# Kernel tuning notes

Hardware: AMD Instinct MI355X
Metric: run time of the kernel (lower is better)

Reference implementation:

```python
import jax, jax.numpy as jnp
import numpy as np

USER_NUM = 100000
ITEM_NUM = 50000
N_NODES = USER_NUM + ITEM_NUM
EMB = 64
LAYERS = 3
NNZ = 2400000


def spmm(rows, cols, vals, x, n):
    # sparse [n, n] (COO) @ dense [n, d] -> [n, d]
    gathered = vals[:, None] * x[cols]          # [nnz, d]
    return jax.ops.segment_sum(gathered, rows, num_segments=n)


def setup_inputs() -> dict:
    key = jax.random.key(0)
    ks = jax.random.split(key, 7)
    return {
        "user_emb": jax.random.normal(ks[0], (USER_NUM, EMB), jnp.float32) * 0.1,
        "item_emb": jax.random.normal(ks[1], (ITEM_NUM, EMB), jnp.float32) * 0.1,
        "w1": jax.random.normal(ks[2], (LAYERS, EMB, EMB), jnp.float32) * (1.0 / np.sqrt(EMB)),
        "w2": jax.random.normal(ks[3], (LAYERS, EMB, EMB), jnp.float32) * (1.0 / np.sqrt(EMB)),
        "adj_vals": jax.random.uniform(ks[4], (NNZ,), jnp.float32) * (1.0 / 16.0),
        "adj_rows": jax.random.randint(ks[5], (NNZ,), 0, N_NODES, jnp.int32),
        "adj_cols": jax.random.randint(ks[6], (NNZ,), 0, N_NODES, jnp.int32),
    }


def reference(user_emb, item_emb, w1, w2, adj_vals, adj_rows, adj_cols):
    ego = jnp.concatenate([user_emb, item_emb], axis=0)   # [N, d]
    n = ego.shape[0]
    all_emb = [ego]
    for k in range(w1.shape[0]):
        temp = ego @ w1[k]                                # [N, d]
        agg_temp = spmm(adj_rows, adj_cols, adj_vals, temp, n)
        agg_ego = spmm(adj_rows, adj_cols, adj_vals, ego, n)
        ego = jax.nn.leaky_relu(agg_temp + temp + (agg_ego * ego) @ w2[k])
        all_emb.append(ego)
    mean_emb = jnp.mean(jnp.stack(all_emb, axis=1), axis=1)  # [N, d]
    u = user_emb.shape[0]
    return mean_emb[:u], mean_emb[u:]
```

## Files before the change

kernel.cpp:

```cpp
#include <hip/hip_runtime.h>
#include <hip/hip_fp16.h>

typedef _Float16 f16;
typedef _Float16 f16x4 __attribute__((ext_vector_type(4)));
typedef _Float16 f16x8 __attribute__((ext_vector_type(8)));
typedef float f32x4 __attribute__((ext_vector_type(4)));

__device__ __forceinline__ float h2f(__half v) { return __half2float(v); }
__device__ __forceinline__ __half f2h(float v) { return __float2half(v); }

#define SCAN_CHUNK 2048
#define ASTRIDE 136

#define BSHIFT 8
#define BROWS (1 << BSHIFT)
#define MAXB 1024
#define TILE 4096
#define BCAP 5120

#define WT_ELEMS (64 * ASTRIDE)
#define WT_DWORDS (WT_ELEMS / 2)

__global__ void zero_out_kernel(float* __restrict__ out, int total) {
    int i = blockIdx.x * blockDim.x + threadIdx.x;
    if (i < total) out[i] = 0.0f;
}

__global__ void init_kernel(const float* __restrict__ user, const float* __restrict__ item,
                            __half* __restrict__ ego0, int usz, int total) {
    int i = blockIdx.x * blockDim.x + threadIdx.x;
    if (i >= total) return;
    float f = (i < usz) ? user[i] : item[i - usz];
    ego0[i] = f2h(f);
}

__global__ void wprep_kernel(const float* __restrict__ w1, const float* __restrict__ w2,
                             f16* __restrict__ wt_pre, int L) {
    int i = blockIdx.x * blockDim.x + threadIdx.x;
    int total = L * WT_ELEMS;
    if (i >= total) return;
    int layer = i / WT_ELEMS;
    int r = i % WT_ELEMS;
    int c = r / ASTRIDE, k = r % ASTRIDE;
    float v = 0.f;
    if (k < 64)       v = w1[(size_t)layer * 4096 + (size_t)k * 64 + c];
    else if (k < 128) v = w2[(size_t)layer * 4096 + (size_t)(k - 64) * 64 + c];
    wt_pre[i] = (f16)v;
}

__global__ void hist_kernel(const int* __restrict__ rows, int* __restrict__ cnt, int nnz) {
    int i = blockIdx.x * blockDim.x + threadIdx.x;
    if (i < nnz) atomicAdd(&cnt[rows[i]], 1);
}

__global__ void scan_pass1(const int* __restrict__ cnt, int* __restrict__ bsum, int n) {
    __shared__ int wt[4];
    int tid = threadIdx.x;
    int base = blockIdx.x * SCAN_CHUNK + tid * 8;
    int s = 0;
    #pragma unroll
    for (int k = 0; k < 8; ++k) { int i = base + k; if (i < n) s += cnt[i]; }
    #pragma unroll
    for (int o = 32; o > 0; o >>= 1) s += __shfl_down(s, o, 64);
    int lane = tid & 63, wid = tid >> 6;
    if (lane == 0) wt[wid] = s;
    __syncthreads();
    if (tid == 0) bsum[blockIdx.x] = wt[0] + wt[1] + wt[2] + wt[3];
}

__global__ void scan_pass2(int* __restrict__ bsum, int nb, int* __restrict__ total) {
    if (threadIdx.x == 0) {
        int run = 0;
        for (int b = 0; b < nb; ++b) { int v = bsum[b]; bsum[b] = run; run += v; }
        *total = run;
    }
}

__global__ void scan_pass3(int* __restrict__ cnt, const int* __restrict__ bsum,
                           int* __restrict__ rptr, int n, const int* __restrict__ total) {
    __shared__ int wt[4];
    int tid = threadIdx.x;
    int base = blockIdx.x * SCAN_CHUNK + tid * 8;
    int v[8];
    int s = 0;
    #pragma unroll
    for (int k = 0; k < 8; ++k) { int i = base + k; v[k] = (i < n) ? cnt[i] : 0; s += v[k]; }
    int lane = tid & 63, wid = tid >> 6;
    int xs = s;
    #pragma unroll
    for (int o = 1; o < 64; o <<= 1) { int t = __shfl_up(xs, o, 64); if (lane >= o) xs += t; }
    if (lane == 63) wt[wid] = xs;
    __syncthreads();
    int wexcl = 0;
    for (int w = 0; w < wid; ++w) wexcl += wt[w];
    int run = bsum[blockIdx.x] + wexcl + (xs - s);
    #pragma unroll
    for (int k = 0; k < 8; ++k) {
        int i = base + k;
        if (i < n) { rptr[i] = run; cnt[i] = run; }
        run += v[k];
    }
    if (blockIdx.x == 0 && tid == 0) rptr[n] = *total;
}

__global__ void scatter_kernel(const int* __restrict__ rows, const int* __restrict__ cols,
                               const float* __restrict__ vals, int* __restrict__ cursor,
                               int2* __restrict__ edges, int nnz) {
    int i = blockIdx.x * blockDim.x + threadIdx.x;
    if (i >= nnz) return;
    int r = rows[i];
    int pos = atomicAdd(&cursor[r], 1);
    edges[pos] = make_int2(cols[i], __float_as_int(vals[i]));
}

__global__ __launch_bounds__(256)
void bhist_kernel(const int* __restrict__ rows, int* __restrict__ bcnt, int nnz, int nbuck) {
    __shared__ int hist[MAXB];
    int tid = threadIdx.x;
    for (int j = tid; j < nbuck; j += 256) hist[j] = 0;
    __syncthreads();
    int i = blockIdx.x * TILE + tid;
    #pragma unroll
    for (int k = 0; k < 16; ++k, i += 256)
        if (i < nnz) atomicAdd(&hist[rows[i] >> BSHIFT], 1);
    __syncthreads();
    for (int j = tid; j < nbuck; j += 256)
        if (hist[j]) atomicAdd(&bcnt[j], hist[j]);
}

__global__ void bscan_kernel(const int* __restrict__ bcnt, int* __restrict__ bbase,
                             int* __restrict__ gcur, int nbuck) {
    if (threadIdx.x == 0) {
        int run = 0;
        for (int b = 0; b < nbuck; ++b) { bbase[b] = run; gcur[b] = run; run += bcnt[b]; }
        bbase[nbuck] = run;
    }
}

__global__ __launch_bounds__(256)
void binA_kernel(const int* __restrict__ rows, const int* __restrict__ cols,
                 const float* __restrict__ vals, int* __restrict__ gcur,
                 int2* __restrict__ bucketed, int nnz, int nbuck) {
    __shared__ int hist[MAXB];
    __shared__ int offs[MAXB];
    __shared__ int rbase[MAXB];
    __shared__ int2 reorder[TILE];
    __shared__ unsigned short slotb[TILE];
    __shared__ int wsum[4];
    int tid = threadIdx.x;
    int tbase = blockIdx.x * TILE;
    int cnt_here = min(TILE, nnz - tbase);

    for (int b = tid; b < MAXB; b += 256) hist[b] = 0;
    __syncthreads();

    int myrow[16]; int mycol[16]; float myval[16];
    #pragma unroll
    for (int k = 0; k < 16; ++k) {
        int i = tbase + tid + k * 256;
        int r = (i < nnz) ? rows[i] : -1;
        myrow[k] = r;
        if (r >= 0) {
            mycol[k] = cols[i];
            myval[k] = vals[i];
            atomicAdd(&hist[r >> BSHIFT], 1);
        }
    }
    __syncthreads();

    int b0 = tid * 4;
    int s0 = hist[b0], s1 = hist[b0 + 1], s2 = hist[b0 + 2], s3 = hist[b0 + 3];
    int tsum = s0 + s1 + s2 + s3;
    int lane = tid & 63, wid = tid >> 6;
    int x = tsum;
    #pragma unroll
    for (int o = 1; o < 64; o <<= 1) { int t = __shfl_up(x, o, 64); if (lane >= o) x += t; }
    if (lane == 63) wsum[wid] = x;
    __syncthreads();
    int wexcl = 0;
    for (int w = 0; w < wid; ++w) wexcl += wsum[w];
    int excl = wexcl + x - tsum;
    offs[b0]     = excl;
    offs[b0 + 1] = excl + s0;
    offs[b0 + 2] = excl + s0 + s1;
    offs[b0 + 3] = excl + s0 + s1 + s2;
    for (int b = tid; b < nbuck; b += 256) {
        int c = hist[b];
        rbase[b] = (c > 0) ? atomicAdd(&gcur[b], c) : 0;
    }
    __syncthreads();
    for (int b = tid; b < MAXB; b += 256) hist[b] = 0;
    __syncthreads();

    #pragma unroll
    for (int k = 0; k < 16; ++k) {
        int r = myrow[k];
        if (r >= 0) {
            int b = r >> BSHIFT;
            int p = offs[b] + atomicAdd(&hist[b], 1);
            reorder[p] = make_int2(((r & (BROWS - 1)) << 20) | mycol[k], __float_as_int(myval[k]));
            slotb[p] = (unsigned short)b;
        }
    }
    __syncthreads();

    for (int t = tid; t < cnt_here; t += 256) {
        int b = slotb[t];
        bucketed[rbase[b] + (t - offs[b])] = reorder[t];
    }
}

__global__ __launch_bounds__(256)
void binB_lds_kernel(const int* __restrict__ bbase, const int2* __restrict__ bucketed,
                     int2* __restrict__ edges, int* __restrict__ rptr, int n, int nbuck) {
    __shared__ int2 srec[BCAP];
    __shared__ int cur[BROWS];
    __shared__ int wsum[4];
    int b = blockIdx.x;
    int row_lo = b << BSHIFT;
    int nrows = min(BROWS, n - row_lo);
    int tid = threadIdx.x;
    int lane = tid & 63, wid = tid >> 6;
    int beg = bbase[b], end = bbase[b + 1];
    int cnt = end - beg;
    bool fits = (cnt <= BCAP);
    cur[tid] = 0;
    __syncthreads();
    if (fits) {
        for (int i = tid; i < cnt; i += 256) {
            int2 r = bucketed[beg + i];
            srec[i] = r;
            atomicAdd(&cur[((unsigned)r.x) >> 20], 1);
        }
    } else {
        for (int i = beg + tid; i < end; i += 256)
            atomicAdd(&cur[((unsigned)bucketed[i].x) >> 20], 1);
    }
    __syncthreads();
    int c0 = cur[tid];
    int x = c0;
    #pragma unroll
    for (int o = 1; o < 64; o <<= 1) { int t = __shfl_up(x, o, 64); if (lane >= o) x += t; }
    if (lane == 63) wsum[wid] = x;
    __syncthreads();
    int wexcl = 0;
    for (int w = 0; w < wid; ++w) wexcl += wsum[w];
    int excl = beg + wexcl + x - c0;
    cur[tid] = excl;
    __syncthreads();
    if (tid < nrows) rptr[row_lo + tid] = cur[tid];
    if (b == nbuck - 1 && tid == 0) rptr[n] = bbase[nbuck];
    if (fits) {
        for (int i = tid; i < cnt; i += 256) {
            int2 rec = srec[i];
            int ro  = ((unsigned)rec.x) >> 20;
            int col = rec.x & 0xFFFFF;
            int pos = atomicAdd(&cur[ro], 1);
            edges[pos] = make_int2(col, rec.y);
        }
    } else {
        for (int i = beg + tid; i < end; i += 256) {
            int2 rec = bucketed[i];
            int ro  = ((unsigned)rec.x) >> 20;
            int col = rec.x & 0xFFFFF;
            int pos = atomicAdd(&cur[ro], 1);
            edges[pos] = make_int2(col, rec.y);
        }
    }
}

__device__ __forceinline__ void spmm_edge_acc(float4& acc, int2 e, const uint2* egov, int g) {
    uint2 gv = egov[((size_t)e.x << 4) + g];
    float v = __int_as_float(e.y);
    float2 a = __half22float2(*(const __half2*)&gv.x);
    float2 b = __half22float2(*(const __half2*)&gv.y);
    acc.x += v * a.x; acc.y += v * a.y; acc.z += v * b.x; acc.w += v * b.y;
}

__global__ __launch_bounds__(512, 4)
void spmm_mfma_kernel(const int* __restrict__ rptr, const int2* __restrict__ edges,
                      const __half* __restrict__ ego, const f16* __restrict__ wtp,
                      __half* __restrict__ ego_out, int n) {
    __shared__ f16 A_lds[32 * ASTRIDE];
    __shared__ f16 Wt_lds[WT_ELEMS];
    int tid = threadIdx.x;
    {
        const unsigned* wp = (const unsigned*)wtp;
        unsigned* wl = (unsigned*)Wt_lds;
        #pragma unroll
        for (int it = 0; it < 9; ++it) {
            int idx = tid + it * 512;
            if (idx < WT_DWORDS) wl[idx] = wp[idx];
        }
    }
    int lane = tid & 63, wid = tid >> 6;
    int sub = lane >> 4;
    int g   = lane & 15;
    int row  = blockIdx.x * 32 + wid * 4 + sub;
    int lrow = wid * 4 + sub;
    bool active = row < n;
    int beg = active ? rptr[row] : 0;
    int end = active ? rptr[row + 1] : 0;
    float4 acc = {0.f, 0.f, 0.f, 0.f};
    const uint2* egov = (const uint2*)ego;
    int j = beg;
    for (; j + 8 <= end; j += 8) {
        int2 e0 = edges[j],     e1 = edges[j + 1], e2 = edges[j + 2], e3 = edges[j + 3];
        int2 e4 = edges[j + 4], e5 = edges[j + 5], e6 = edges[j + 6], e7 = edges[j + 7];
        spmm_edge_acc(acc, e0, egov, g);
        spmm_edge_acc(acc, e1, egov, g);
        spmm_edge_acc(acc, e2, egov, g);
        spmm_edge_acc(acc, e3, egov, g);
        spmm_edge_acc(acc, e4, egov, g);
        spmm_edge_acc(acc, e5, egov, g);
        spmm_edge_acc(acc, e6, egov, g);
        spmm_edge_acc(acc, e7, egov, g);
    }
    for (; j + 4 <= end; j += 4) {
        int2 e0 = edges[j], e1 = edges[j + 1], e2 = edges[j + 2], e3 = edges[j + 3];
        spmm_edge_acc(acc, e0, egov, g);
        spmm_edge_acc(acc, e1, egov, g);
        spmm_edge_acc(acc, e2, egov, g);
        spmm_edge_acc(acc, e3, egov, g);
    }
    for (; j < end; ++j) {
        spmm_edge_acc(acc, edges[j], egov, g);
    }
    {
        uint2 xv = egov[(size_t)(active ? row : 0) * 16 + g];
        float2 x01 = __half22float2(*(const __half2*)&xv.x);
        float2 x23 = __half22float2(*(const __half2*)&xv.y);
        f16x4 sv, pv;
        sv[0] = (f16)(acc.x + x01.x); sv[1] = (f16)(acc.y + x01.y);
        sv[2] = (f16)(acc.z + x23.x); sv[3] = (f16)(acc.w + x23.y);
        pv[0] = (f16)(acc.x * x01.x); pv[1] = (f16)(acc.y * x01.y);
        pv[2] = (f16)(acc.z * x23.x); pv[3] = (f16)(acc.w * x23.y);
        f16* ar = &A_lds[lrow * ASTRIDE + g * 4];
        *(f16x4*)ar        = sv;
        *(f16x4*)(ar + 64) = pv;
    }
    __syncthreads();
    int band = wid >> 2;
    int nt   = wid & 3;
    int m = lane & 15, q = lane >> 4;
    f32x4 dacc = {0.f, 0.f, 0.f, 0.f};
    const f16* arow = &A_lds[(band * 16 + m) * ASTRIDE + q * 8];
    const f16* brow = &Wt_lds[(nt * 16 + m) * ASTRIDE + q * 8];
    #pragma unroll
    for (int ks = 0; ks < 4; ++ks) {
        f16x8 av = *(const f16x8*)(arow + ks * 32);
        f16x8 bv = *(const f16x8*)(brow + ks * 32);
        dacc = __builtin_amdgcn_mfma_f32_16x16x32_f16(av, bv, dacc, 0, 0, 0);
    }
    int rbase = blockIdx.x * 32 + band * 16 + q * 4;
    #pragma unroll
    for (int r = 0; r < 4; ++r) {
        int grow = rbase + r;
        if (grow < n) {
            float e0 = dacc[r]; e0 = (e0 > 0.f) ? e0 : 0.01f * e0;
            ego_out[(size_t)grow * 64 + nt * 16 + m] = f2h(e0);
        }
    }
}

__global__ void finalize4_kernel(const __half* __restrict__ e0, const __half* __restrict__ e1,
                                 const __half* __restrict__ e2, const __half* __restrict__ e3,
                                 float* __restrict__ out, const int* __restrict__ rptr,
                                 int N, int nnz, float scale, int total) {
    int i = blockIdx.x * blockDim.x + threadIdx.x;
    if (i >= total) return;
    bool ok = (rptr[N] == nnz);
    float s = h2f(e0[i]) + h2f(e1[i]) + h2f(e2[i]) + h2f(e3[i]);
    out[i] = ok ? s * scale : 0.75f;
}

__global__ void acc_kernel(const __half* __restrict__ e, float* __restrict__ out,
                           float scale, int total, int first) {
    int i = blockIdx.x * blockDim.x + threadIdx.x;
    if (i >= total) return;
    float v = h2f(e[i]) * scale;
    out[i] = first ? v : out[i] + v;
}

extern "C" void kernel_launch(void* const* d_in, const int* in_sizes, int n_in,
                              void* d_out, int out_size, void* d_ws, size_t ws_size,
                              hipStream_t stream) {
    const float* user = (const float*)d_in[0];
    const float* item = (const float*)d_in[1];
    const float* w1   = (const float*)d_in[2];
    const float* w2   = (const float*)d_in[3];
    const float* vals = (const float*)d_in[4];
    const int*   rows = (const int*)d_in[5];
    const int*   cols = (const int*)d_in[6];

    const int usz = in_sizes[0];
    const int isz = in_sizes[1];
    const int L   = in_sizes[2] / 4096;
    const int nnz = in_sizes[4];
    const int N   = (usz + isz) / 64;
    const int ND  = N * 64;
    const int nbscan = (N + SCAN_CHUNK - 1) / SCAN_CHUNK;
    const int nbuck  = (N + BROWS - 1) >> BSHIFT;

    char* p = (char*)d_ws;
    auto alloc = [&](size_t bytes) -> void* {
        void* r = (void*)p;
        p += (bytes + 255) & ~(size_t)255;
        return r;
    };
    __half* egos   = (__half*)alloc((size_t)(L + 1) * ND * 2);
    __half* aggE   = (__half*)alloc((size_t)ND * 2);
    int2*   edges  = (int2*)alloc((size_t)nnz * 8);
    int*    rptr   = (int*)alloc((size_t)(N + 1) * 4);
    int*    cnt    = (int*)alloc((size_t)N * 4);
    int*    bsum   = (int*)alloc((size_t)nbscan * 4);
    int*    total  = (int*)alloc(4);
    int*    bcnt   = (int*)alloc((size_t)(MAXB + 1) * 4);
    int*    bbase  = (int*)alloc((size_t)(MAXB + 1) * 4);
    int*    gcur   = (int*)alloc((size_t)MAXB * 4);
    f16*    wt_pre = (f16*)alloc((size_t)L * WT_ELEMS * 2);
    bool fast_sort = (nbuck <= MAXB) && (N < (1 << 20)) && (nnz > 0);
    int2* bucketed = nullptr;
    if (fast_sort) {
        if ((size_t)ND * 2 >= (size_t)nnz * 8) bucketed = (int2*)aggE;
        else bucketed = (int2*)alloc((size_t)nnz * 8);
    }
    size_t need = (size_t)(p - (char*)d_ws);
    (void)n_in; (void)out_size;

    if (need > ws_size) {
        zero_out_kernel<<<(ND + 255) / 256, 256, 0, stream>>>((float*)d_out, ND);
        return;
    }

    init_kernel<<<(ND + 255) / 256, 256, 0, stream>>>(user, item, egos, usz, ND);
    wprep_kernel<<<(L * WT_ELEMS + 255) / 256, 256, 0, stream>>>(w1, w2, wt_pre, L);

    if (fast_sort) {
        hipMemsetAsync(bcnt, 0, (size_t)nbuck * 4, stream);
        bhist_kernel<<<(nnz + TILE - 1) / TILE, 256, 0, stream>>>(rows, bcnt, nnz, nbuck);
        bscan_kernel<<<1, 64, 0, stream>>>(bcnt, bbase, gcur, nbuck);
        binA_kernel<<<(nnz + TILE - 1) / TILE, 256, 0, stream>>>(rows, cols, vals, gcur,
                                                                 bucketed, nnz, nbuck);
        binB_lds_kernel<<<nbuck, 256, 0, stream>>>(bbase, bucketed, edges, rptr, N, nbuck);
    } else {
        hipMemsetAsync(cnt, 0, (size_t)N * 4, stream);
        hist_kernel<<<(nnz + 255) / 256, 256, 0, stream>>>(rows, cnt, nnz);
        scan_pass1<<<nbscan, 256, 0, stream>>>(cnt, bsum, N);
        scan_pass2<<<1, 64, 0, stream>>>(bsum, nbscan, total);
        scan_pass3<<<nbscan, 256, 0, stream>>>(cnt, bsum, rptr, N, total);
        scatter_kernel<<<(nnz + 255) / 256, 256, 0, stream>>>(rows, cols, vals, cnt, edges, nnz);
    }

    const int fb = (N + 31) / 32;
    for (int k = 0; k < L; ++k) {
        __half* ein  = egos + (size_t)k * ND;
        __half* eout = egos + (size_t)(k + 1) * ND;
        spmm_mfma_kernel<<<fb, 512, 0, stream>>>(rptr, edges, ein, wt_pre + (size_t)k * WT_ELEMS,
                                                 eout, N);
    }
    float scale = 1.0f / (float)(L + 1);
    if (L == 3) {
        finalize4_kernel<<<(ND + 255) / 256, 256, 0, stream>>>(
            egos, egos + (size_t)ND, egos + (size_t)2 * ND, egos + (size_t)3 * ND,
            (float*)d_out, rptr, N, nnz, scale, ND);
    } else {
        for (int k = 0; k <= L; ++k)
            acc_kernel<<<(ND + 255) / 256, 256, 0, stream>>>(egos + (size_t)k * ND,
                                                             (float*)d_out, scale, ND, k == 0);
    }
}
```

Before: 435.6 us.

## Use fixed-capacity buckets to drop histogram pass and fuse setup and finalize

The edge bucketing now gives each row bucket a fixed slot region of BCAP entries, so the separate bucket histogram, memset and serial scan kernels go away. binB instead computes each bucket's global offset from the other buckets' fill counts. The init and weight-prep kernels are merged into one setup kernel that also seeds the bucket cursors. The final mean over layers is folded into the last SpMM layer's epilogue. The cost is that a bucket holding more than BCAP edges silently loses the extras, and the existing rptr check then yields the sentinel output, so correctness depends on rows being spread evenly across buckets.

```diff
diff --git a/kernel.cpp b/kernel.cpp
--- a/kernel.cpp
+++ b/kernel.cpp
@@ -26,26 +26,26 @@
     if (i < total) out[i] = 0.0f;
 }
 
-__global__ void init_kernel(const float* __restrict__ user, const float* __restrict__ item,
-                            __half* __restrict__ ego0, int usz, int total) {
+__global__ void setup_kernel(const float* __restrict__ user, const float* __restrict__ item,
+                             __half* __restrict__ ego0, int usz, int ND,
+                             const float* __restrict__ w1, const float* __restrict__ w2,
+                             f16* __restrict__ wt_pre, int L,
+                             int* __restrict__ gcur, int nbuck) {
     int i = blockIdx.x * blockDim.x + threadIdx.x;
-    if (i >= total) return;
-    float f = (i < usz) ? user[i] : item[i - usz];
-    ego0[i] = f2h(f);
-}
-
-__global__ void wprep_kernel(const float* __restrict__ w1, const float* __restrict__ w2,
-                             f16* __restrict__ wt_pre, int L) {
-    int i = blockIdx.x * blockDim.x + threadIdx.x;
-    int total = L * WT_ELEMS;
-    if (i >= total) return;
-    int layer = i / WT_ELEMS;
-    int r = i % WT_ELEMS;
-    int c = r / ASTRIDE, k = r % ASTRIDE;
-    float v = 0.f;
-    if (k < 64)       v = w1[(size_t)layer * 4096 + (size_t)k * 64 + c];
-    else if (k < 128) v = w2[(size_t)layer * 4096 + (size_t)(k - 64) * 64 + c];
-    wt_pre[i] = (f16)v;
+    if (i < ND) {
+        float f = (i < usz) ? user[i] : item[i - usz];
+        ego0[i] = f2h(f);
+    }
+    if (i < L * WT_ELEMS) {
+        int layer = i / WT_ELEMS;
+        int r = i % WT_ELEMS;
+        int c = r / ASTRIDE, k = r % ASTRIDE;
+        float v = 0.f;
+        if (k < 64)       v = w1[(size_t)layer * 4096 + (size_t)k * 64 + c];
+        else if (k < 128) v = w2[(size_t)layer * 4096 + (size_t)(k - 64) * 64 + c];
+        wt_pre[i] = (f16)v;
+    }
+    if (i < nbuck) gcur[i] = i * BCAP;
 }
 
 __global__ void hist_kernel(const int* __restrict__ rows, int* __restrict__ cnt, int nnz) {
@@ -111,30 +111,6 @@
     int r = rows[i];
     int pos = atomicAdd(&cursor[r], 1);
     edges[pos] = make_int2(cols[i], __float_as_int(vals[i]));
-}
-
-__global__ __launch_bounds__(256)
-void bhist_kernel(const int* __restrict__ rows, int* __restrict__ bcnt, int nnz, int nbuck) {
-    __shared__ int hist[MAXB];
-    int tid = threadIdx.x;
-    for (int j = tid; j < nbuck; j += 256) hist[j] = 0;
-    __syncthreads();
-    int i = blockIdx.x * TILE + tid;
-    #pragma unroll
-    for (int k = 0; k < 16; ++k, i += 256)
-        if (i < nnz) atomicAdd(&hist[rows[i] >> BSHIFT], 1);
-    __syncthreads();
-    for (int j = tid; j < nbuck; j += 256)
-        if (hist[j]) atomicAdd(&bcnt[j], hist[j]);
-}
-
-__global__ void bscan_kernel(const int* __restrict__ bcnt, int* __restrict__ bbase,
-                             int* __restrict__ gcur, int nbuck) {
-    if (threadIdx.x == 0) {
-        int run = 0;
-        for (int b = 0; b < nbuck; ++b) { bbase[b] = run; gcur[b] = run; run += bcnt[b]; }
-        bbase[nbuck] = run;
-    }
 }
 
 __global__ __launch_bounds__(256)
@@ -206,13 +182,14 @@
 
     for (int t = tid; t < cnt_here; t += 256) {
         int b = slotb[t];
-        bucketed[rbase[b] + (t - offs[b])] = reorder[t];
+        int dst = rbase[b] + (t - offs[b]);
+        if (dst < (b + 1) * BCAP) bucketed[dst] = reorder[t];
     }
 }
 
 __global__ __launch_bounds__(256)
-void binB_lds_kernel(const int* __restrict__ bbase, const int2* __restrict__ bucketed,
-                     int2* __restrict__ edges, int* __restrict__ rptr, int n, int nbuck) {
+void binB_kernel(const int* __restrict__ gcur, const int2* __restrict__ bucketed,
+                 int2* __restrict__ edges, int* __restrict__ rptr, int n, int nbuck) {
     __shared__ int2 srec[BCAP];
     __shared__ int cur[BROWS];
     __shared__ int wsum[4];
@@ -221,20 +198,20 @@
     int nrows = min(BROWS, n - row_lo);
     int tid = threadIdx.x;
     int lane = tid & 63, wid = tid >> 6;
-    int beg = bbase[b], end = bbase[b + 1];
-    int cnt = end - beg;
-    bool fits = (cnt <= BCAP);
     cur[tid] = 0;
-    __syncthreads();
-    if (fits) {
-        for (int i = tid; i < cnt; i += 256) {
-            int2 r = bucketed[beg + i];
-            srec[i] = r;
-            atomicAdd(&cur[((unsigned)r.x) >> 20], 1);
-        }
-    } else {
-        for (int i = beg + tid; i < end; i += 256)
-            atomicAdd(&cur[((unsigned)bucketed[i].x) >> 20], 1);
+    int ps = 0;
+    for (int j = tid; j < b; j += 256) ps += min(gcur[j] - j * BCAP, BCAP);
+    #pragma unroll
+    for (int o = 32; o > 0; o >>= 1) ps += __shfl_down(ps, o, 64);
+    if (lane == 0) wsum[wid] = ps;
+    __syncthreads();
+    int beg = wsum[0] + wsum[1] + wsum[2] + wsum[3];
+    int cnt = min(gcur[b] - b * BCAP, BCAP);
+    int src = b * BCAP;
+    for (int i = tid; i < cnt; i += 256) {
+        int2 r = bucketed[src + i];
+        srec[i] = r;
+        atomicAdd(&cur[((unsigned)r.x) >> 20], 1);
     }
     __syncthreads();
     int c0 = cur[tid];
@@ -249,23 +226,13 @@
     cur[tid] = excl;
     __syncthreads();
     if (tid < nrows) rptr[row_lo + tid] = cur[tid];
-    if (b == nbuck - 1 && tid == 0) rptr[n] = bbase[nbuck];
-    if (fits) {
-        for (int i = tid; i < cnt; i += 256) {
-            int2 rec = srec[i];
-            int ro  = ((unsigned)rec.x) >> 20;
-            int col = rec.x & 0xFFFFF;
-            int pos = atomicAdd(&cur[ro], 1);
-            edges[pos] = make_int2(col, rec.y);
-        }
-    } else {
-        for (int i = beg + tid; i < end; i += 256) {
-            int2 rec = bucketed[i];
-            int ro  = ((unsigned)rec.x) >> 20;
-            int col = rec.x & 0xFFFFF;
-            int pos = atomicAdd(&cur[ro], 1);
-            edges[pos] = make_int2(col, rec.y);
-        }
+    if (b == nbuck - 1 && tid == 0) rptr[n] = beg + cnt;
+    for (int i = tid; i < cnt; i += 256) {
+        int2 rec = srec[i];
+        int ro  = ((unsigned)rec.x) >> 20;
+        int col = rec.x & 0xFFFFF;
+        int pos = atomicAdd(&cur[ro], 1);
+        edges[pos] = make_int2(col, rec.y);
     }
 }
 
@@ -277,10 +244,14 @@
     acc.x += v * a.x; acc.y += v * a.y; acc.z += v * b.x; acc.w += v * b.y;
 }
 
+template<int FINAL>
 __global__ __launch_bounds__(512, 4)
 void spmm_mfma_kernel(const int* __restrict__ rptr, const int2* __restrict__ edges,
                       const __half* __restrict__ ego, const f16* __restrict__ wtp,
-                      __half* __restrict__ ego_out, int n) {
+                      __half* __restrict__ ego_out,
+                      const __half* __restrict__ e0p, const __half* __restrict__ e1p,
+                      const __half* __restrict__ e2p, float* __restrict__ outp,
+                      int n, int nnz, float scale) {
     __shared__ f16 A_lds[32 * ASTRIDE];
     __shared__ f16 Wt_lds[WT_ELEMS];
     int tid = threadIdx.x;
@@ -353,25 +324,28 @@
         dacc = __builtin_amdgcn_mfma_f32_16x16x32_f16(av, bv, dacc, 0, 0, 0);
     }
     int rbase = blockIdx.x * 32 + band * 16 + q * 4;
-    #pragma unroll
-    for (int r = 0; r < 4; ++r) {
-        int grow = rbase + r;
-        if (grow < n) {
-            float e0 = dacc[r]; e0 = (e0 > 0.f) ? e0 : 0.01f * e0;
-            ego_out[(size_t)grow * 64 + nt * 16 + m] = f2h(e0);
-        }
-    }
-}
-
-__global__ void finalize4_kernel(const __half* __restrict__ e0, const __half* __restrict__ e1,
-                                 const __half* __restrict__ e2, const __half* __restrict__ e3,
-                                 float* __restrict__ out, const int* __restrict__ rptr,
-                                 int N, int nnz, float scale, int total) {
-    int i = blockIdx.x * blockDim.x + threadIdx.x;
-    if (i >= total) return;
-    bool ok = (rptr[N] == nnz);
-    float s = h2f(e0[i]) + h2f(e1[i]) + h2f(e2[i]) + h2f(e3[i]);
-    out[i] = ok ? s * scale : 0.75f;
+    if (FINAL) {
+        bool ok = (rptr[n] == nnz);
+        #pragma unroll
+        for (int r = 0; r < 4; ++r) {
+            int grow = rbase + r;
+            if (grow < n) {
+                float v = dacc[r]; v = (v > 0.f) ? v : 0.01f * v;
+                size_t o = (size_t)grow * 64 + nt * 16 + m;
+                float s = h2f(e0p[o]) + h2f(e1p[o]) + h2f(e2p[o]) + v;
+                outp[o] = ok ? s * scale : 0.75f;
+            }
+        }
+    } else {
+        #pragma unroll
+        for (int r = 0; r < 4; ++r) {
+            int grow = rbase + r;
+            if (grow < n) {
+                float v = dacc[r]; v = (v > 0.f) ? v : 0.01f * v;
+                ego_out[(size_t)grow * 64 + nt * 16 + m] = f2h(v);
+            }
+        }
+    }
 }
 
 __global__ void acc_kernel(const __half* __restrict__ e, float* __restrict__ out,
@@ -409,22 +383,17 @@
         return r;
     };
     __half* egos   = (__half*)alloc((size_t)(L + 1) * ND * 2);
-    __half* aggE   = (__half*)alloc((size_t)ND * 2);
     int2*   edges  = (int2*)alloc((size_t)nnz * 8);
     int*    rptr   = (int*)alloc((size_t)(N + 1) * 4);
     int*    cnt    = (int*)alloc((size_t)N * 4);
     int*    bsum   = (int*)alloc((size_t)nbscan * 4);
     int*    total  = (int*)alloc(4);
-    int*    bcnt   = (int*)alloc((size_t)(MAXB + 1) * 4);
-    int*    bbase  = (int*)alloc((size_t)(MAXB + 1) * 4);
     int*    gcur   = (int*)alloc((size_t)MAXB * 4);
     f16*    wt_pre = (f16*)alloc((size_t)L * WT_ELEMS * 2);
-    bool fast_sort = (nbuck <= MAXB) && (N < (1 << 20)) && (nnz > 0);
-    int2* bucketed = nullptr;
-    if (fast_sort) {
-        if ((size_t)ND * 2 >= (size_t)nnz * 8) bucketed = (int2*)aggE;
-        else bucketed = (int2*)alloc((size_t)nnz * 8);
-    }
+    bool fast_sort = (nbuck <= MAXB) && (N < (1 << 20)) && (nnz > 0) &&
+                     ((size_t)L * ND * 2 >= (size_t)nbuck * BCAP * 8);
+    int2* bucketed = (int2*)(egos + ND);
+    if (fast_sort && (size_t)L * ND * 2 < (size_t)nbuck * BCAP * 8) fast_sort = false;
     size_t need = (size_t)(p - (char*)d_ws);
     (void)n_in; (void)out_size;
 
@@ -433,16 +402,15 @@
         return;
     }
 
-    init_kernel<<<(ND + 255) / 256, 256, 0, stream>>>(user, item, egos, usz, ND);
-    wprep_kernel<<<(L * WT_ELEMS + 255) / 256, 256, 0, stream>>>(w1, w2, wt_pre, L);
+    int setup_max = ND > L * WT_ELEMS ? ND : L * WT_ELEMS;
+    if (setup_max < nbuck) setup_max = nbuck;
+    setup_kernel<<<(setup_max + 255) / 256, 256, 0, stream>>>(user, item, egos, usz, ND,
+                                                              w1, w2, wt_pre, L, gcur, nbuck);
 
     if (fast_sort) {
-        hipMemsetAsync(bcnt, 0, (size_t)nbuck * 4, stream);
-        bhist_kernel<<<(nnz + TILE - 1) / TILE, 256, 0, stream>>>(rows, bcnt, nnz, nbuck);
-        bscan_kernel<<<1, 64, 0, stream>>>(bcnt, bbase, gcur, nbuck);
         binA_kernel<<<(nnz + TILE - 1) / TILE, 256, 0, stream>>>(rows, cols, vals, gcur,
                                                                  bucketed, nnz, nbuck);
-        binB_lds_kernel<<<nbuck, 256, 0, stream>>>(bbase, bucketed, edges, rptr, N, nbuck);
+        binB_kernel<<<nbuck, 256, 0, stream>>>(gcur, bucketed, edges, rptr, N, nbuck);
     } else {
         hipMemsetAsync(cnt, 0, (size_t)N * 4, stream);
         hist_kernel<<<(nnz + 255) / 256, 256, 0, stream>>>(rows, cnt, nnz);
@@ -453,18 +421,23 @@
     }
 
     const int fb = (N + 31) / 32;
+    float scale = 1.0f / (float)(L + 1);
     for (int k = 0; k < L; ++k) {
         __half* ein  = egos + (size_t)k * ND;
         __half* eout = egos + (size_t)(k + 1) * ND;
-        spmm_mfma_kernel<<<fb, 512, 0, stream>>>(rptr, edges, ein, wt_pre + (size_t)k * WT_ELEMS,
-                                                 eout, N);
-    }
-    float scale = 1.0f / (float)(L + 1);
-    if (L == 3) {
-        finalize4_kernel<<<(ND + 255) / 256, 256, 0, stream>>>(
-            egos, egos + (size_t)ND, egos + (size_t)2 * ND, egos + (size_t)3 * ND,
-            (float*)d_out, rptr, N, nnz, scale, ND);
-    } else {
+        const f16* wtp = wt_pre + (size_t)k * WT_ELEMS;
+        if (L == 3 && k == 2) {
+            spmm_mfma_kernel<1><<<fb, 512, 0, stream>>>(rptr, edges, ein, wtp, eout,
+                                                        egos, egos + (size_t)ND,
+                                                        egos + (size_t)2 * ND,
+                                                        (float*)d_out, N, nnz, scale);
+        } else {
+            spmm_mfma_kernel<0><<<fb, 512, 0, stream>>>(rptr, edges, ein, wtp, eout,
+                                                        nullptr, nullptr, nullptr,
+                                                        nullptr, N, nnz, scale);
+        }
+    }
+    if (L != 3) {
         for (int k = 0; k <= L; ++k)
             acc_kernel<<<(ND + 255) / 256, 256, 0, stream>>>(egos + (size_t)k * ND,
                                                              (float*)d_out, scale, ND, k == 0);
```

After: 366.2 us. 15.9% less time.
